# Kernel optimization log

Measured on AMD Instinct MI355X. Metric: run time of the kernel, lower is better.

Reference implementation:

```python
import jax, jax.numpy as jnp
import numpy as np

DIM = 384
HEADS = 12
WS = 7
MLPH = 1536
B = 32
EPS = 1e-5


def _rel_index():
    coords = np.stack(np.meshgrid(np.arange(WS), np.arange(WS), indexing='ij'))  # [2,7,7]
    cf = coords.reshape(2, -1)  # [2,49]
    rel = cf[:, :, None] - cf[:, None, :]  # [2,49,49]
    rel = rel.transpose(1, 2, 0).astype(np.int64)
    rel[:, :, 0] += WS - 1
    rel[:, :, 1] += WS - 1
    rel[:, :, 0] *= 2 * WS - 1
    return jnp.asarray(rel.sum(-1), dtype=jnp.int32)  # [49,49]


def setup_inputs() -> dict:
    key = jax.random.key(0)
    ks = jax.random.split(key, 16)
    H, W = 56, 56
    L = H * W
    s = 0.02
    inp = {
        'x': jax.random.normal(ks[0], (B, L, DIM), jnp.float32),
        'ln1_g': jnp.ones((DIM,), jnp.float32),
        'ln1_b': jnp.zeros((DIM,), jnp.float32),
        'qkv_w': jax.random.normal(ks[1], (DIM, 3 * DIM), jnp.float32) * s,
        'qkv_b': jnp.zeros((3 * DIM,), jnp.float32),
        'rpb_table': jax.random.normal(ks[2], ((2 * WS - 1) ** 2, HEADS), jnp.float32) * s,
        'proj_w': jax.random.normal(ks[3], (DIM, DIM), jnp.float32) * s,
        'proj_b': jnp.zeros((DIM,), jnp.float32),
        'ln2_g': jnp.ones((DIM,), jnp.float32),
        'ln2_b': jnp.zeros((DIM,), jnp.float32),
        'mlp_w1': jax.random.normal(ks[4], (DIM, MLPH), jnp.float32) * s,
        'mlp_b1': jnp.zeros((MLPH,), jnp.float32),
        'mlp_w2': jax.random.normal(ks[5], (MLPH, DIM), jnp.float32) * s,
        'mlp_b2': jnp.zeros((DIM,), jnp.float32),
        'rel_idx': _rel_index(),
        'H': H,
        'W': W,
    }
    return inp


def _ln(x, g, b):
    m = jnp.mean(x, axis=-1, keepdims=True)
    v = jnp.mean(jnp.square(x - m), axis=-1, keepdims=True)
    return (x - m) * jax.lax.rsqrt(v + EPS) * g + b


def reference(x, ln1_g, ln1_b, qkv_w, qkv_b, rpb_table, proj_w, proj_b,
              ln2_g, ln2_b, mlp_w1, mlp_b1, mlp_w2, mlp_b2, rel_idx, H, W):
    Bb, L, C = x.shape
    N = WS * WS
    hd = C // HEADS
    scale = hd ** -0.5

    shortcut = x
    h = _ln(x, ln1_g, ln1_b).reshape(Bb, H, W, C)
    # window partition -> [nW, 49, C]
    h = h.reshape(Bb, H // WS, WS, W // WS, WS, C).transpose(0, 1, 3, 2, 4, 5)
    wins = h.reshape(-1, N, C)
    nW = wins.shape[0]

    qkv = (wins @ qkv_w + qkv_b).reshape(nW, N, 3, HEADS, hd).transpose(2, 0, 3, 1, 4)
    q, k, v = qkv[0] * scale, qkv[1], qkv[2]  # [nW, heads, 49, hd]

    attn = jnp.einsum('bhnd,bhmd->bhnm', q, k)
    bias = rpb_table[rel_idx].transpose(2, 0, 1)  # [heads,49,49]
    attn = jax.nn.softmax(attn + bias[None], axis=-1)
    out = jnp.einsum('bhnm,bhmd->bhnd', attn, v).transpose(0, 2, 1, 3).reshape(nW, N, C)
    out = out @ proj_w + proj_b

    # window reverse -> [B, L, C]
    out = out.reshape(Bb, H // WS, W // WS, WS, WS, C).transpose(0, 1, 3, 2, 4, 5).reshape(Bb, L, C)

    x = shortcut + out
    h2 = _ln(x, ln2_g, ln2_b)
    mlp = jax.nn.gelu(h2 @ mlp_w1 + mlp_b1, approximate=False) @ mlp_w2 + mlp_b2
    return x + mlp
```

## Files before the change

### kernel.cpp

```cpp
#include <hip/hip_runtime.h>
#include <hip/hip_bf16.h>
#include <cstdint>
#include <cstddef>

#define HEADS 12
#define LL 3136
#define ROWS 100352
#define SCALE 0.17677669529663687f

typedef __hip_bfloat16 bf16;
typedef __attribute__((ext_vector_type(8))) short short8;
typedef __attribute__((ext_vector_type(4))) short s4;
typedef __attribute__((ext_vector_type(4))) float f32x4;

__device__ __forceinline__ float bf2f(unsigned short u) {
  union { uint32_t u32; float f; } x; x.u32 = ((uint32_t)u) << 16; return x.f;
}
__device__ __forceinline__ unsigned short f2bf_bits(float f) {
  union { float f; uint32_t u; } x; x.f = f;
  uint32_t r = x.u + 0x7fffu + ((x.u >> 16) & 1u);
  return (unsigned short)(r >> 16);
}

__global__ __launch_bounds__(256) void prep_transpose(const float* __restrict__ src,
    bf16* __restrict__ dst, int K, int N, int scaleLim, float scale) {
  __shared__ float tile[64][65];
  const int kb = blockIdx.x * 64, nb = blockIdx.y * 64;
  const int tx = threadIdx.x & 63;
  const int ty = threadIdx.x >> 6;
  #pragma unroll
  for (int i = 0; i < 16; ++i) {
    int k = ty * 16 + i;
    tile[k][tx] = src[(size_t)(kb + k) * N + nb + tx];
  }
  __syncthreads();
  #pragma unroll
  for (int i = 0; i < 16; ++i) {
    int n = ty * 16 + i;
    float v = tile[tx][n];
    if (nb + n < scaleLim) v *= scale;
    dst[(size_t)(nb + n) * K + kb + tx] = __float2bfloat16(v);
  }
}

__global__ void prep_qb(const float* __restrict__ qkv_b, float* __restrict__ qb) {
  int idx = blockIdx.x * 256 + threadIdx.x;
  if (idx < 1152) qb[idx] = qkv_b[idx] * (idx < 384 ? SCALE : 1.0f);
}

__global__ void prep_biasM(const float* __restrict__ rpb, const int* __restrict__ rel,
                           f32x4* __restrict__ biasM) {
  int h = blockIdx.x;
  int t = blockIdx.y;
  int mi = t >> 2, ni = t & 3;
  int lane = threadIdx.x;
  int q = ni * 16 + (lane & 15);
  int g = lane >> 4;
  f32x4 v;
  #pragma unroll
  for (int j = 0; j < 4; ++j) {
    int k = mi * 16 + g * 4 + j;
    float b;
    if (k < 49) b = (q < 49) ? rpb[rel[q * 49 + k] * HEADS + h] : 0.f;
    else        b = -1e30f;
    v[j] = b;
  }
  biasM[((h * 4 + mi) * 4 + ni) * 64 + lane] = v;
}

template<bool WIN>
__global__ __launch_bounds__(256) void ln_kernel(const float* __restrict__ x,
    const float* __restrict__ g, const float* __restrict__ b, bf16* __restrict__ out) {
  int row = blockIdx.x * 4 + (threadIdx.x >> 6);
  int lane = threadIdx.x & 63;
  size_t src;
  if (WIN) {
    int w = row / 49, p = row - w * 49;
    int bb = w >> 6, wy = (w >> 3) & 7, wx = w & 7;
    int iy = p / 7, ix = p - iy * 7;
    int l = (wy * 7 + iy) * 56 + wx * 7 + ix;
    src = ((size_t)bb * LL + l) * 384;
  } else {
    src = (size_t)row * 384;
  }
  const float* xr = x + src;
  float vals[6];
  float s = 0.f, s2 = 0.f;
  #pragma unroll
  for (int j = 0; j < 6; ++j) {
    float v = xr[lane + 64 * j];
    vals[j] = v; s += v; s2 += v * v;
  }
  #pragma unroll
  for (int off = 32; off >= 1; off >>= 1) {
    s  += __shfl_xor(s, off);
    s2 += __shfl_xor(s2, off);
  }
  float m  = s * (1.f / 384.f);
  float var = s2 * (1.f / 384.f) - m * m;
  float rs = rsqrtf(var + 1e-5f);
  bf16* orow = out + (size_t)row * 384;
  #pragma unroll
  for (int j = 0; j < 6; ++j) {
    int c = lane + 64 * j;
    orow[c] = __float2bfloat16((vals[j] - m) * rs * g[c] + b[c]);
  }
}

template<int EPI>
__global__ __launch_bounds__(256) void gemm_bt(const bf16* __restrict__ A,
    const bf16* __restrict__ Bt, const float* __restrict__ bias,
    bf16* __restrict__ Cb, float* __restrict__ Cf, const float* __restrict__ resid,
    int M, int N, int K) {
  __shared__ bf16 lsA[3][128 * 32];
  __shared__ bf16 lsB[3][128 * 32];
  const int t = threadIdx.x;
  const int lane = t & 63;
  const int wave = t >> 6;
  const int wm = wave >> 1, wn = wave & 1;
  const int lrow = lane & 15;
  const int lk = (lane >> 4) * 8;
  const int n0 = blockIdx.x * 128;
  const int m0 = blockIdx.y * 128;

  f32x4 acc[4][4];
  #pragma unroll
  for (int i = 0; i < 4; ++i)
    #pragma unroll
    for (int j = 0; j < 4; ++j) acc[i][j] = (f32x4){0.f, 0.f, 0.f, 0.f};

  auto stage = [&](int buf, int tile) {
    int k0 = tile * 32;
    #pragma unroll
    for (int i = 0; i < 2; ++i) {
      int e = (i * 256 + t) * 8;
      int r = e >> 5, c = e & 31;
      const bf16* ga = A  + (size_t)(m0 + r) * K + (k0 + c);
      const bf16* gb = Bt + (size_t)(n0 + r) * K + (k0 + c);
      __builtin_amdgcn_global_load_lds((const __attribute__((address_space(1))) void*)ga,
          (__attribute__((address_space(3))) void*)&lsA[buf][e], 16, 0, 0);
      __builtin_amdgcn_global_load_lds((const __attribute__((address_space(1))) void*)gb,
          (__attribute__((address_space(3))) void*)&lsB[buf][e], 16, 0, 0);
    }
  };

  auto compute = [&](int buf) {
    short8 af[4], bfr[4];
    #pragma unroll
    for (int mi = 0; mi < 4; ++mi)
      af[mi] = *(const short8*)&lsA[buf][(wm * 64 + mi * 16 + lrow) * 32 + lk];
    #pragma unroll
    for (int ni = 0; ni < 4; ++ni)
      bfr[ni] = *(const short8*)&lsB[buf][(wn * 64 + ni * 16 + lrow) * 32 + lk];
    #pragma unroll
    for (int mi = 0; mi < 4; ++mi)
      #pragma unroll
      for (int ni = 0; ni < 4; ++ni)
        acc[mi][ni] = __builtin_amdgcn_mfma_f32_16x16x32_bf16(af[mi], bfr[ni], acc[mi][ni], 0, 0, 0);
  };

  const int nt = K >> 5;
  stage(0, 0);
  if (nt > 1) stage(1, 1);
  int cur = 0, pre = 2;
  for (int it = 0; it < nt; ++it) {
    __builtin_amdgcn_s_barrier();
    if (it + 2 < nt) stage(pre, it + 2);
    int rem = nt - 1 - it;
    if (rem >= 2)      asm volatile("s_waitcnt vmcnt(8)" ::: "memory");
    else if (rem == 1) asm volatile("s_waitcnt vmcnt(4)" ::: "memory");
    else               asm volatile("s_waitcnt vmcnt(0)" ::: "memory");
    __builtin_amdgcn_s_barrier();
    compute(cur);
    pre = cur;
    cur = (cur == 2) ? 0 : cur + 1;
  }

  #pragma unroll
  for (int mi = 0; mi < 4; ++mi) {
    #pragma unroll
    for (int ni = 0; ni < 4; ++ni) {
      int col = n0 + wn * 64 + ni * 16 + lrow;
      float bv = bias[col];
      #pragma unroll
      for (int j = 0; j < 4; ++j) {
        int row = m0 + wm * 64 + mi * 16 + (lane >> 4) * 4 + j;
        float v = acc[mi][ni][j] + bv;
        if constexpr (EPI == 0) {
          Cb[(size_t)row * N + col] = __float2bfloat16(v);
        } else if constexpr (EPI == 1) {
          v = v * 0.5f * (1.0f + erff(v * 0.70710678118654752f));
          Cb[(size_t)row * N + col] = __float2bfloat16(v);
        } else if constexpr (EPI == 2) {
          int w = row / 49, p = row - w * 49;
          int bb = w >> 6, wy = (w >> 3) & 7, wx = w & 7;
          int iy = p / 7, ix = p - iy * 7;
          int l = (wy * 7 + iy) * 56 + wx * 7 + ix;
          size_t di = ((size_t)bb * LL + l) * 384 + col;
          Cf[di] = v + resid[di];
        } else {
          size_t di = (size_t)row * N + col;
          Cf[di] = v + resid[di];
        }
      }
    }
  }
}

__global__ __launch_bounds__(256) void attn_mfma(const bf16* __restrict__ qkv,
    const f32x4* __restrict__ biasM, bf16* __restrict__ out) {
  __shared__ __align__(16) short lds4[4][6272];
  const int wv = threadIdx.x >> 6;
  const int lane = threadIdx.x & 63;
  const int w = blockIdx.x * 4 + wv;
  const int h = blockIdx.y;
  short* L = &lds4[wv][0];
  const short* base = (const short*)(qkv + (size_t)w * 49 * 1152 + h * 32);

  #pragma unroll
  for (int i = 0; i < 4; ++i) {
    int t = i * 64 + lane;
    int r = t >> 2, c = t & 3;
    short8 qv, kv, vv;
    if (r < 49) {
      const short* rp = base + (size_t)r * 1152;
      qv = *(const short8*)(rp + c * 8);
      kv = *(const short8*)(rp + 384 + c * 8);
      vv = *(const short8*)(rp + 768 + c * 8);
    } else {
      qv = (short8)0; kv = (short8)0; vv = (short8)0;
    }
    *(short8*)&L[r * 32 + c * 8] = kv;
    *(short8*)&L[2048 + r * 32 + c * 8] = qv;
    #pragma unroll
    for (int j = 0; j < 8; ++j) L[4096 + (c * 8 + j) * 68 + r] = vv[j];
  }

  const int g = lane >> 4, r15 = lane & 15;

  short8 ka[4], qb[4];
  #pragma unroll
  for (int mi = 0; mi < 4; ++mi)
    ka[mi] = *(const short8*)&L[(mi * 16 + r15) * 32 + g * 8];
  #pragma unroll
  for (int ni = 0; ni < 4; ++ni)
    qb[ni] = *(const short8*)&L[2048 + (ni * 16 + r15) * 32 + g * 8];

  f32x4 sT[4][4];
  #pragma unroll
  for (int mi = 0; mi < 4; ++mi)
    #pragma unroll
    for (int ni = 0; ni < 4; ++ni)
      sT[mi][ni] = biasM[((h * 4 + mi) * 4 + ni) * 64 + lane];
  #pragma unroll
  for (int mi = 0; mi < 4; ++mi)
    #pragma unroll
    for (int ni = 0; ni < 4; ++ni)
      sT[mi][ni] = __builtin_amdgcn_mfma_f32_16x16x32_bf16(ka[mi], qb[ni], sT[mi][ni], 0, 0, 0);

  float inv_[4];
  #pragma unroll
  for (int ni = 0; ni < 4; ++ni) {
    float m = -1e30f;
    #pragma unroll
    for (int mi = 0; mi < 4; ++mi)
      #pragma unroll
      for (int j = 0; j < 4; ++j) m = fmaxf(m, sT[mi][ni][j]);
    m = fmaxf(m, __shfl_xor(m, 16));
    m = fmaxf(m, __shfl_xor(m, 32));
    float s = 0.f;
    #pragma unroll
    for (int mi = 0; mi < 4; ++mi)
      #pragma unroll
      for (int j = 0; j < 4; ++j) {
        float p = __expf(sT[mi][ni][j] - m);
        sT[mi][ni][j] = p; s += p;
      }
    s += __shfl_xor(s, 16);
    s += __shfl_xor(s, 32);
    inv_[ni] = 1.f / s;
  }

  s4 pa[4][4];
  #pragma unroll
  for (int mi = 0; mi < 4; ++mi)
    #pragma unroll
    for (int ni = 0; ni < 4; ++ni) {
      s4 p;
      #pragma unroll
      for (int j = 0; j < 4; ++j)
        p[j] = (short)f2bf_bits(sT[mi][ni][j] * inv_[ni]);
      pa[mi][ni] = p;
    }

  s4 vb[4][2];
  #pragma unroll
  for (int mi = 0; mi < 4; ++mi)
    #pragma unroll
    for (int di = 0; di < 2; ++di)
      vb[mi][di] = *(const s4*)&L[4096 + (di * 16 + r15) * 68 + mi * 16 + g * 4];

  f32x4 o[4][2];
  #pragma unroll
  for (int ni = 0; ni < 4; ++ni)
    #pragma unroll
    for (int di = 0; di < 2; ++di) o[ni][di] = (f32x4){0.f, 0.f, 0.f, 0.f};

  asm volatile("s_nop 3" ::: );
  #pragma unroll
  for (int ni = 0; ni < 4; ++ni)
    #pragma unroll
    for (int di = 0; di < 2; ++di)
      #pragma unroll
      for (int mi = 0; mi < 4; ++mi) {
#if __has_builtin(__builtin_amdgcn_mfma_f32_16x16x16bf16_1k)
        o[ni][di] = __builtin_amdgcn_mfma_f32_16x16x16bf16_1k(pa[mi][ni], vb[mi][di], o[ni][di], 0, 0, 0);
#else
        asm volatile("v_mfma_f32_16x16x16_bf16 %0, %1, %2, %0"
                     : "+v"(o[ni][di]) : "v"(pa[mi][ni]), "v"(vb[mi][di]));
#endif
      }
  asm volatile("s_nop 7\n\ts_nop 7" ::: );

  bf16* op = out + ((size_t)w * 49) * 384 + h * 32;
  #pragma unroll
  for (int ni = 0; ni < 4; ++ni)
    #pragma unroll
    for (int di = 0; di < 2; ++di)
      #pragma unroll
      for (int j = 0; j < 4; ++j) {
        int q = ni * 16 + g * 4 + j;
        if (q < 49)
          op[(size_t)q * 384 + di * 16 + r15] = __float2bfloat16(o[ni][di][j]);
      }
}

extern "C" void kernel_launch(void* const* d_in, const int* in_sizes, int n_in,
                              void* d_out, int out_size, void* d_ws, size_t ws_size,
                              hipStream_t stream) {
  const float* x      = (const float*)d_in[0];
  const float* ln1_g  = (const float*)d_in[1];
  const float* ln1_b  = (const float*)d_in[2];
  const float* qkv_w  = (const float*)d_in[3];
  const float* qkv_b  = (const float*)d_in[4];
  const float* rpb    = (const float*)d_in[5];
  const float* proj_w = (const float*)d_in[6];
  const float* proj_b = (const float*)d_in[7];
  const float* ln2_g  = (const float*)d_in[8];
  const float* ln2_b  = (const float*)d_in[9];
  const float* mlp_w1 = (const float*)d_in[10];
  const float* mlp_b1 = (const float*)d_in[11];
  const float* mlp_w2 = (const float*)d_in[12];
  const float* mlp_b2 = (const float*)d_in[13];
  const int*   rel    = (const int*)d_in[14];

  char* ws = (char*)d_ws;
  const size_t OFF_WQKV  = 0;
  const size_t OFF_WPROJ = OFF_WQKV + (size_t)1152 * 384 * 2;
  const size_t OFF_WM1   = OFF_WPROJ + (size_t)384 * 384 * 2;
  const size_t OFF_WM2   = OFF_WM1 + (size_t)1536 * 384 * 2;
  const size_t OFF_QB    = OFF_WM2 + (size_t)384 * 1536 * 2;
  const size_t OFF_HWIN  = 3659776;
  const size_t OFF_QKV   = OFF_HWIN + (size_t)ROWS * 384 * 2;
  const size_t OFF_ATTN  = OFF_QKV + (size_t)ROWS * 1152 * 2;
  const size_t OFF_X2    = OFF_ATTN + (size_t)ROWS * 384 * 2;
  const size_t OFF_M1    = OFF_QKV;
  const size_t OFF_H2    = OFF_HWIN;
  const size_t OFF_BIASM = OFF_X2;

  bf16*  wqkv  = (bf16*)(ws + OFF_WQKV);
  bf16*  wproj = (bf16*)(ws + OFF_WPROJ);
  bf16*  wm1   = (bf16*)(ws + OFF_WM1);
  bf16*  wm2   = (bf16*)(ws + OFF_WM2);
  float* qb    = (float*)(ws + OFF_QB);
  f32x4* biasM = (f32x4*)(ws + OFF_BIASM);
  bf16*  hwin  = (bf16*)(ws + OFF_HWIN);
  bf16*  qkvb  = (bf16*)(ws + OFF_QKV);
  bf16*  attnb = (bf16*)(ws + OFF_ATTN);
  float* x2    = (float*)(ws + OFF_X2);
  bf16*  m1    = (bf16*)(ws + OFF_M1);
  bf16*  h2    = (bf16*)(ws + OFF_H2);
  float* outp  = (float*)d_out;

  prep_transpose<<<dim3(384 / 64, 1152 / 64), 256, 0, stream>>>(qkv_w, wqkv, 384, 1152, 384, SCALE);
  prep_transpose<<<dim3(384 / 64, 384 / 64), 256, 0, stream>>>(proj_w, wproj, 384, 384, 0, 1.f);
  prep_transpose<<<dim3(384 / 64, 1536 / 64), 256, 0, stream>>>(mlp_w1, wm1, 384, 1536, 0, 1.f);
  prep_transpose<<<dim3(1536 / 64, 384 / 64), 256, 0, stream>>>(mlp_w2, wm2, 1536, 384, 0, 1.f);
  prep_qb<<<5, 256, 0, stream>>>(qkv_b, qb);
  prep_biasM<<<dim3(12, 16), 64, 0, stream>>>(rpb, rel, biasM);

  ln_kernel<true><<<ROWS / 4, 256, 0, stream>>>(x, ln1_g, ln1_b, hwin);
  gemm_bt<0><<<dim3(1152 / 128, ROWS / 128), 256, 0, stream>>>(
      hwin, wqkv, qb, qkvb, nullptr, nullptr, ROWS, 1152, 384);
  attn_mfma<<<dim3(512, HEADS), 256, 0, stream>>>(qkvb, biasM, attnb);
  gemm_bt<2><<<dim3(384 / 128, ROWS / 128), 256, 0, stream>>>(
      attnb, wproj, proj_b, nullptr, x2, x, ROWS, 384, 384);
  ln_kernel<false><<<ROWS / 4, 256, 0, stream>>>(x2, ln2_g, ln2_b, h2);
  gemm_bt<1><<<dim3(1536 / 128, ROWS / 128), 256, 0, stream>>>(
      h2, wm1, mlp_b1, m1, nullptr, nullptr, ROWS, 1536, 384);
  gemm_bt<3><<<dim3(384 / 128, ROWS / 128), 256, 0, stream>>>(
      m1, wm2, mlp_b2, nullptr, outp, x2, ROWS, 384, 1536);
}
```

Measured before the change: 960.7 us.

## Load GEMM B fragments directly from global, double-buffer A, remap blocks per XCD

The GEMM no longer stages the weight operand through LDS. Each wave loads its B fragments straight from global memory into registers, one k-tile ahead. The A operand moves from triple to double buffering with a simpler syncthreads pipeline. The launch becomes a 1D grid with a remapping that spreads consecutive tiles across the 8 XCDs, aiming at better L2 locality and lower LDS use for higher occupancy. The risks are uncoalesced, latency-exposed B loads and shallower prefetch of A.

```diff
diff --git a/kernel.cpp b/kernel.cpp
--- a/kernel.cpp
+++ b/kernel.cpp
@@ -112,16 +112,19 @@
     const bf16* __restrict__ Bt, const float* __restrict__ bias,
     bf16* __restrict__ Cb, float* __restrict__ Cf, const float* __restrict__ resid,
     int M, int N, int K) {
-  __shared__ bf16 lsA[3][128 * 32];
-  __shared__ bf16 lsB[3][128 * 32];
+  __shared__ bf16 lsA[2][128 * 32];
   const int t = threadIdx.x;
   const int lane = t & 63;
   const int wave = t >> 6;
   const int wm = wave >> 1, wn = wave & 1;
   const int lrow = lane & 15;
   const int lk = (lane >> 4) * 8;
-  const int n0 = blockIdx.x * 128;
-  const int m0 = blockIdx.y * 128;
+  const int nbx = N >> 7;
+  const int nwg = (M >> 7) * nbx;
+  const int cpx = nwg >> 3;
+  const int id2 = (blockIdx.x & 7) * cpx + (blockIdx.x >> 3);
+  const int n0 = (id2 % nbx) * 128;
+  const int m0 = (id2 / nbx) * 128;
 
   f32x4 acc[4][4];
   #pragma unroll
@@ -129,29 +132,29 @@
     #pragma unroll
     for (int j = 0; j < 4; ++j) acc[i][j] = (f32x4){0.f, 0.f, 0.f, 0.f};
 
-  auto stage = [&](int buf, int tile) {
+  auto stageA = [&](int buf, int tile) {
     int k0 = tile * 32;
     #pragma unroll
     for (int i = 0; i < 2; ++i) {
       int e = (i * 256 + t) * 8;
       int r = e >> 5, c = e & 31;
-      const bf16* ga = A  + (size_t)(m0 + r) * K + (k0 + c);
-      const bf16* gb = Bt + (size_t)(n0 + r) * K + (k0 + c);
+      const bf16* ga = A + (size_t)(m0 + r) * K + (k0 + c);
       __builtin_amdgcn_global_load_lds((const __attribute__((address_space(1))) void*)ga,
           (__attribute__((address_space(3))) void*)&lsA[buf][e], 16, 0, 0);
-      __builtin_amdgcn_global_load_lds((const __attribute__((address_space(1))) void*)gb,
-          (__attribute__((address_space(3))) void*)&lsB[buf][e], 16, 0, 0);
     }
   };
 
-  auto compute = [&](int buf) {
-    short8 af[4], bfr[4];
+  auto loadB = [&](int k0, short8* dst) {
+    #pragma unroll
+    for (int ni = 0; ni < 4; ++ni)
+      dst[ni] = *(const short8*)(Bt + (size_t)(n0 + wn * 64 + ni * 16 + lrow) * K + k0 + lk);
+  };
+
+  auto computeA = [&](int buf, const short8* bfr) {
+    short8 af[4];
     #pragma unroll
     for (int mi = 0; mi < 4; ++mi)
       af[mi] = *(const short8*)&lsA[buf][(wm * 64 + mi * 16 + lrow) * 32 + lk];
-    #pragma unroll
-    for (int ni = 0; ni < 4; ++ni)
-      bfr[ni] = *(const short8*)&lsB[buf][(wn * 64 + ni * 16 + lrow) * 32 + lk];
     #pragma unroll
     for (int mi = 0; mi < 4; ++mi)
       #pragma unroll
@@ -160,20 +163,23 @@
   };
 
   const int nt = K >> 5;
-  stage(0, 0);
-  if (nt > 1) stage(1, 1);
-  int cur = 0, pre = 2;
+  short8 b0[4], b1[4];
+  stageA(0, 0);
+  loadB(0, b0);
+  __syncthreads();
+  int cur = 0;
   for (int it = 0; it < nt; ++it) {
-    __builtin_amdgcn_s_barrier();
-    if (it + 2 < nt) stage(pre, it + 2);
-    int rem = nt - 1 - it;
-    if (rem >= 2)      asm volatile("s_waitcnt vmcnt(8)" ::: "memory");
-    else if (rem == 1) asm volatile("s_waitcnt vmcnt(4)" ::: "memory");
-    else               asm volatile("s_waitcnt vmcnt(0)" ::: "memory");
-    __builtin_amdgcn_s_barrier();
-    compute(cur);
-    pre = cur;
-    cur = (cur == 2) ? 0 : cur + 1;
+    if (it + 1 < nt) {
+      stageA(cur ^ 1, it + 1);
+      loadB((it + 1) * 32, b1);
+    }
+    computeA(cur, b0);
+    __syncthreads();
+    if (it + 1 < nt) {
+      #pragma unroll
+      for (int i = 0; i < 4; ++i) b0[i] = b1[i];
+    }
+    cur ^= 1;
   }
 
   #pragma unroll
@@ -390,14 +396,14 @@
   prep_biasM<<<dim3(12, 16), 64, 0, stream>>>(rpb, rel, biasM);
 
   ln_kernel<true><<<ROWS / 4, 256, 0, stream>>>(x, ln1_g, ln1_b, hwin);
-  gemm_bt<0><<<dim3(1152 / 128, ROWS / 128), 256, 0, stream>>>(
+  gemm_bt<0><<<(1152 / 128) * (ROWS / 128), 256, 0, stream>>>(
       hwin, wqkv, qb, qkvb, nullptr, nullptr, ROWS, 1152, 384);
   attn_mfma<<<dim3(512, HEADS), 256, 0, stream>>>(qkvb, biasM, attnb);
-  gemm_bt<2><<<dim3(384 / 128, ROWS / 128), 256, 0, stream>>>(
+  gemm_bt<2><<<(384 / 128) * (ROWS / 128), 256, 0, stream>>>(
       attnb, wproj, proj_b, nullptr, x2, x, ROWS, 384, 384);
   ln_kernel<false><<<ROWS / 4, 256, 0, stream>>>(x2, ln2_g, ln2_b, h2);
-  gemm_bt<1><<<dim3(1536 / 128, ROWS / 128), 256, 0, stream>>>(
+  gemm_bt<1><<<(1536 / 128) * (ROWS / 128), 256, 0, stream>>>(
       h2, wm1, mlp_b1, m1, nullptr, nullptr, ROWS, 1536, 384);
-  gemm_bt<3><<<dim3(384 / 128, ROWS / 128), 256, 0, stream>>>(
+  gemm_bt<3><<<(384 / 128) * (ROWS / 128), 256, 0, stream>>>(
       m1, wm2, mlp_b2, nullptr, outp, x2, ROWS, 384, 1536);
 }
```

Result: slower. 1.171 ms (+21.9%).
